# Optimization experiments

Hardware: AMD Instinct MI355X
Metric: run time of the kernel (lower is better)

## Reference

```python
import jax, jax.numpy as jnp
import numpy as np

DIM = 96
D_STATE = 16
EXPAND = 2
D_INNER = EXPAND * DIM
DT_RANK = (DIM + 15) // 16  # 6
B, H, W = 2, 64, 64
K = 4  # scan directions


def _ln(x, w, b, eps=1e-5):
    mu = x.mean(-1, keepdims=True)
    var = x.var(-1, keepdims=True)
    return (x - mu) / jnp.sqrt(var + eps) * w + b


def setup_inputs() -> dict:
    key = jax.random.key(0)
    ks = jax.random.split(key, 10)
    f = jnp.float32
    x = jax.random.normal(ks[0], (B, H, W, DIM), dtype=f)
    y = jax.random.normal(ks[1], (B, H, W, DIM), dtype=f)
    inp = {
        'x': x,
        'y': y,
        'ln_w': jnp.ones((DIM,), f),
        'ln_b': jnp.zeros((DIM,), f),
        'in_proj_w': jax.random.normal(ks[2], (2 * D_INNER, DIM), f) * 0.05,
        'conv_w': jax.random.normal(ks[3], (D_INNER, 1, 3, 3), f) * 0.1,
        'conv_b': jnp.zeros((D_INNER,), f),
        'x_proj_w': jax.random.normal(ks[4], (K, DT_RANK + 2 * D_STATE, D_INNER), f) * 0.05,
        'dt_w': jax.random.normal(ks[5], (K, D_INNER, DT_RANK), f) * 0.1,
        'dt_b': jax.random.normal(ks[6], (K, D_INNER), f) * 0.1,
        'A_log': jnp.broadcast_to(jnp.log(jnp.arange(1, D_STATE + 1, dtype=f)), (K, D_INNER, D_STATE)),
        'Ds': jnp.ones((K, D_INNER), f),
        'out_norm_w': jnp.ones((D_INNER,), f),
        'out_norm_b': jnp.zeros((D_INNER,), f),
        'out_proj_w': jax.random.normal(ks[7], (DIM, D_INNER), f) * 0.05,
    }
    return inp


def _fwd(x, y, ln_w, ln_b, in_proj_w, conv_w, conv_b, x_proj_w, dt_w, dt_b,
         A_log, Ds, out_norm_w, out_norm_b, out_proj_w):
    Bsz, Hh, Ww, C = x.shape
    Din = conv_w.shape[0]
    N = A_log.shape[-1]
    R = dt_w.shape[-1]
    L = Hh * Ww

    diff = jnp.abs(x - y)                       # TemporalSpectrumBlock abs-diff
    h = _ln(diff, ln_w, ln_b)                   # VSSBlock ln_1
    xz = h @ in_proj_w.T                        # (B,H,W,2*Din)
    xm, z = jnp.split(xz, 2, axis=-1)
    xm = xm.transpose(0, 3, 1, 2)               # (B,Din,H,W)
    xm = jax.lax.conv_general_dilated(
        xm, conv_w, (1, 1), 'SAME', feature_group_count=Din,
        dimension_numbers=('NCHW', 'OIHW', 'NCHW')) + conv_b[None, :, None, None]
    xm = jax.nn.silu(xm)

    # 4-directional sequences (B,4,Din,L)
    x0 = xm.reshape(Bsz, Din, L)
    x1 = xm.transpose(0, 1, 3, 2).reshape(Bsz, Din, L)
    xs = jnp.stack([x0, x1], axis=1)
    xs = jnp.concatenate([xs, jnp.flip(xs, axis=-1)], axis=1)

    x_dbl = jnp.einsum('bkdl,kcd->bkcl', xs, x_proj_w)
    dts, Bs, Cs = jnp.split(x_dbl, [R, R + N], axis=2)   # (B,4,R,L),(B,4,N,L),(B,4,N,L)
    dts = jnp.einsum('bkrl,kdr->bkdl', dts, dt_w)
    delta = jax.nn.softplus(dts + dt_b[None, :, :, None])  # (B,4,Din,L)

    A = -jnp.exp(A_log)                                    # (4,Din,N)
    dA = jnp.exp(delta[..., None] * A[None, :, :, None, :])          # (B,4,Din,L,N)
    dBu = delta[..., None] * Bs.transpose(0, 1, 3, 2)[:, :, None] * xs[..., None]

    dA_t = dA.transpose(3, 0, 1, 2, 4)    # (L,B,4,Din,N)
    dBu_t = dBu.transpose(3, 0, 1, 2, 4)
    C_t = Cs.transpose(3, 0, 1, 2)        # (L,B,4,N)
    h0 = jnp.zeros((Bsz, 4, Din, N), dtype=x.dtype)

    def step(hc, inp):
        a, bu, c = inp
        hc = a * hc + bu
        yv = jnp.einsum('bkdn,bkn->bkd', hc, c)
        return hc, yv

    _, ys = jax.lax.scan(step, h0, (dA_t, dBu_t, C_t))    # (L,B,4,Din)
    ys = ys.transpose(1, 2, 3, 0)                          # (B,4,Din,L)
    out_y = ys + Ds[None, :, :, None] * xs

    inv_y = jnp.flip(out_y[:, 2:4], axis=-1)
    wh_y = out_y[:, 1].reshape(Bsz, Din, Ww, Hh).transpose(0, 1, 3, 2).reshape(Bsz, Din, L)
    invwh_y = inv_y[:, 1].reshape(Bsz, Din, Ww, Hh).transpose(0, 1, 3, 2).reshape(Bsz, Din, L)
    yc = out_y[:, 0] + inv_y[:, 0] + wh_y + invwh_y        # (B,Din,L)
    yc = yc.transpose(0, 2, 1).reshape(Bsz, Hh, Ww, Din)

    yn = _ln(yc, out_norm_w, out_norm_b)
    out = (yn * jax.nn.silu(z)) @ out_proj_w.T
    return diff + out                                      # residual around the block


def reference(x, y, ln_w, ln_b, in_proj_w, conv_w, conv_b, x_proj_w, dt_w, dt_b,
              A_log, Ds, out_norm_w, out_norm_b, out_proj_w):
    return _fwd(x, y, ln_w, ln_b, in_proj_w, conv_w, conv_b, x_proj_w, dt_w, dt_b,
                A_log, Ds, out_norm_w, out_norm_b, out_proj_w)
```

## Files before the change

### kernel.cpp

```cpp
#include <hip/hip_runtime.h>
#include <math.h>

#define DIMC 96
#define DIN  192
#define NST  16
#define RNK  6
#define KD   4
#define HH   64
#define WWD  64
#define LL   4096
#define BB   2
#define NC   64
#define CH   64

__device__ __forceinline__ int pos_of(int k, int l) {
    int t = ((l & 63) << 6) | (l >> 6);
    switch (k) {
        case 0: return l;
        case 1: return t;
        case 2: return LL - 1 - l;
        default: return ((((LL-1-l) & 63) << 6) | ((LL-1-l) >> 6));
    }
}

__device__ __forceinline__ float silu_f(float v) {
    return v / (1.f + expf(-v));
}

__global__ __launch_bounds__(256) void k0_prep(
    const float* __restrict__ Win, const float* __restrict__ Wout,
    const float* __restrict__ xpw,
    float* __restrict__ WinT, float* __restrict__ WoutT, float* __restrict__ xpwT)
{
    int idx = blockIdx.x*256 + threadIdx.x;
    int stride = gridDim.x*256;
    for (int i = idx; i < 96*384; i += stride) {
        int j = i / 384, o = i - j*384;
        WinT[i] = Win[o*96 + j];
    }
    for (int i = idx; i < 192*96; i += stride) {
        int j = i / 96, o = i - j*96;
        WoutT[i] = Wout[o*192 + j];
    }
    for (int i = idx; i < 4*192*40; i += stride) {
        int kk = i / 7680; int rem = i - kk*7680;
        int j = rem / 40, c = rem - j*40;
        xpwT[i] = (c < RNK + 2*NST) ? xpw[((size_t)kk*(RNK+2*NST) + c)*DIN + j] : 0.f;
    }
}

__global__ __launch_bounds__(256) void k1_ln_inproj(
    const float* __restrict__ x, const float* __restrict__ y,
    const float* __restrict__ lnw, const float* __restrict__ lnb,
    const float* __restrict__ WinT,
    float* __restrict__ diff, float* __restrict__ xm, float* __restrict__ zbuf)
{
    __shared__ float hT[96*36];
    __shared__ float wl[96*132];
    __shared__ float mu_s[32], rs_s[32];
    int t = threadIdx.x;
    int p0 = blockIdx.x * 32;

    #pragma unroll
    for (int s = 0; s < 12; s++) {
        int i = t + 256*s;
        float v = fabsf(x[(size_t)p0*96 + i] - y[(size_t)p0*96 + i]);
        diff[(size_t)p0*96 + i] = v;
        int pos = i / 96, ch = i - pos*96;
        hT[ch*36 + pos] = v;
    }
    __syncthreads();
    {
        int tg = t & 7, pos = t >> 3;
        float s1 = 0.f, s2 = 0.f;
        #pragma unroll
        for (int m = 0; m < 12; m++) {
            float v = hT[(tg + 8*m)*36 + pos];
            s1 += v; s2 += v*v;
        }
        s1 += __shfl_down(s1, 4, 8); s2 += __shfl_down(s2, 4, 8);
        s1 += __shfl_down(s1, 2, 8); s2 += __shfl_down(s2, 2, 8);
        s1 += __shfl_down(s1, 1, 8); s2 += __shfl_down(s2, 1, 8);
        if (tg == 0) {
            float mu = s1 * (1.f/96.f);
            float var = s2 * (1.f/96.f) - mu*mu;
            mu_s[pos] = mu; rs_s[pos] = rsqrtf(var + 1e-5f);
        }
    }
    __syncthreads();
    #pragma unroll
    for (int s = 0; s < 12; s++) {
        int i = t + 256*s;
        int pos = i / 96, ch = i - pos*96;
        float v = hT[ch*36 + pos];
        hT[ch*36 + pos] = (v - mu_s[pos]) * rs_s[pos] * lnw[ch] + lnb[ch];
    }

    int o2 = t & 31, pg = t >> 5;
    for (int ot = 0; ot < 3; ot++) {
        __syncthreads();
        #pragma unroll
        for (int s = 0; s < 48; s++) {
            int i = t + 256*s;
            int j = i >> 7, ol = i & 127;
            wl[j*132 + ol] = WinT[j*384 + ot*128 + ol];
        }
        __syncthreads();
        float acc[4][4];
        #pragma unroll
        for (int a = 0; a < 4; a++)
            #pragma unroll
            for (int c = 0; c < 4; c++) acc[a][c] = 0.f;
        #pragma unroll 4
        for (int j = 0; j < 96; j++) {
            float wv[4], hv[4];
            *(float4*)wv = *(const float4*)&wl[j*132 + 4*o2];
            *(float4*)hv = *(const float4*)&hT[j*36 + 4*pg];
            #pragma unroll
            for (int pi = 0; pi < 4; pi++)
                #pragma unroll
                for (int c = 0; c < 4; c++) acc[pi][c] += hv[pi] * wv[c];
        }
        #pragma unroll
        for (int pi = 0; pi < 4; pi++) {
            int pos = p0 + 4*pg + pi;
            float4 val = make_float4(acc[pi][0], acc[pi][1], acc[pi][2], acc[pi][3]);
            int og = ot*128 + 4*o2;
            if (og < 192) *(float4*)&xm[(size_t)pos*192 + og] = val;
            else          *(float4*)&zbuf[(size_t)pos*192 + (og - 192)] = val;
        }
    }
}

__global__ __launch_bounds__(192) void k2_conv(
    const float* __restrict__ xm, const float* __restrict__ cw,
    const float* __restrict__ cb, float* __restrict__ xconv)
{
    int p = blockIdx.x;
    int d = threadIdx.x;
    int b = p >> 12;
    int l = p & (LL - 1);
    int hh = l >> 6, ww = l & 63;
    float acc = cb[d];
    const float* wd = cw + d*9;
    #pragma unroll
    for (int di = -1; di <= 1; di++) {
        int h2 = hh + di;
        if ((unsigned)h2 < HH) {
            #pragma unroll
            for (int dj = -1; dj <= 1; dj++) {
                int w2 = ww + dj;
                if ((unsigned)w2 < WWD)
                    acc += wd[(di+1)*3 + (dj+1)] * xm[((size_t)b*LL + h2*WWD + w2)*DIN + d];
            }
        }
    }
    xconv[(size_t)p*DIN + d] = silu_f(acc);
}

__global__ __launch_bounds__(256) void k3_xproj(
    const float* __restrict__ xconv, const float* __restrict__ xpwT,
    const float* __restrict__ dtw, const float* __restrict__ dtb,
    float* __restrict__ delta, float* __restrict__ Bs, float* __restrict__ Cs)
{
    __shared__ float uT[192*36];
    __shared__ float wx[192*40 + 64];
    __shared__ float xdl[32*40];
    int t = threadIdx.x;
    int blk = blockIdx.x;
    int tile = blk & 127, bk = blk >> 7;
    int k = bk & 3, b = bk >> 2;
    int c0 = tile*32;

    #pragma unroll
    for (int s = 0; s < 24; s++) {
        int i = t + 256*s;
        int pos = i / 192, ch = i - pos*192;
        int pp = pos_of(k, c0 + pos);
        uT[ch*36 + pos] = xconv[((size_t)b*LL + pp)*DIN + ch];
    }
    #pragma unroll
    for (int s = 0; s < 30; s++) {
        int i = t + 256*s;
        wx[i] = xpwT[(size_t)k*7680 + i];
    }
    __syncthreads();

    int pq = t & 7, cg = t >> 3;
    float a0[4] = {0,0,0,0}, a1[4] = {0,0,0,0};
    #pragma unroll 4
    for (int j = 0; j < 192; j++) {
        float uv[4];
        *(float4*)uv = *(const float4*)&uT[j*36 + 4*pq];
        float w0 = wx[j*40 + cg];
        float w1 = wx[j*40 + cg + 32];
        #pragma unroll
        for (int pi = 0; pi < 4; pi++) { a0[pi] += uv[pi]*w0; a1[pi] += uv[pi]*w1; }
    }
    #pragma unroll
    for (int pi = 0; pi < 4; pi++) {
        xdl[(4*pq + pi)*40 + cg] = a0[pi];
        if (cg < 8) xdl[(4*pq + pi)*40 + cg + 32] = a1[pi];
    }
    __syncthreads();

    if (t < 192) {
        int d = t;
        float w6[RNK];
        #pragma unroll
        for (int r = 0; r < RNK; r++) w6[r] = dtw[((size_t)k*DIN + d)*RNK + r];
        float bias = dtb[k*DIN + d];
        for (int pp = 0; pp < 32; pp++) {
            float acc = bias;
            #pragma unroll
            for (int r = 0; r < RNK; r++) acc += xdl[pp*40 + r] * w6[r];
            float sp = (acc > 20.f) ? acc : log1pf(expf(acc));
            delta[((size_t)bk*LL + c0 + pp)*DIN + d] = sp;
        }
    } else {
        int q = t - 192;
        int pp = q >> 1, half = q & 1;
        #pragma unroll
        for (int n8 = 0; n8 < 8; n8++) {
            int n = half*8 + n8;
            Bs[((size_t)bk*LL + c0 + pp)*NST + n] = xdl[pp*40 + RNK + n];
            Cs[((size_t)bk*LL + c0 + pp)*NST + n] = xdl[pp*40 + RNK + NST + n];
        }
    }
}

__global__ __launch_bounds__(192) void k4_scanA(
    const float* __restrict__ xconv, const float* __restrict__ delta,
    const float* __restrict__ BsArr, const float* __restrict__ A_log,
    float* __restrict__ P, float* __restrict__ Q)
{
    int blk = blockIdx.x;
    int c  = blk & (NC - 1);
    int bk = blk >> 6;
    int k  = bk & 3;
    int b  = bk >> 2;
    int d  = threadIdx.x;
    __shared__ float sB[CH][NST];
    for (int i = d; i < CH*NST; i += DIN) {
        int step = i >> 4, n = i & 15;
        sB[step][n] = BsArr[((size_t)bk*LL + c*CH + step)*NST + n];
    }
    float A[NST];
    #pragma unroll
    for (int n = 0; n < NST; n++) A[n] = -expf(A_log[((size_t)k*DIN + d)*NST + n]);
    __syncthreads();

    float h[NST], p[NST];
    #pragma unroll
    for (int n = 0; n < NST; n++) { h[n] = 0.f; p[n] = 1.f; }

    for (int step = 0; step < CH; step++) {
        int l = c*CH + step;
        float dl = delta[((size_t)bk*LL + l)*DIN + d];
        float uu = xconv[((size_t)b*LL + pos_of(k, l))*DIN + d];
        float du = dl * uu;
        #pragma unroll
        for (int n = 0; n < NST; n++) {
            float a = __expf(dl * A[n]);
            h[n] = a*h[n] + du*sB[step][n];
            p[n] *= a;
        }
    }
    size_t base = (size_t)blk*NST*DIN + d;
    #pragma unroll
    for (int n = 0; n < NST; n++) { P[base + n*DIN] = p[n]; Q[base + n*DIN] = h[n]; }
}

__global__ __launch_bounds__(256) void k5_scanB(
    const float* __restrict__ P, float* __restrict__ Q)
{
    int idx = blockIdx.x*256 + threadIdx.x;
    if (idx >= BB*KD*NST*DIN) return;
    int d = idx % DIN;
    int rest = idx / DIN;
    int n = rest % NST; rest /= NST;
    int k = rest % KD;
    int b = rest / KD;
    size_t base = ((((size_t)(b*KD + k))*NC)*NST + n)*DIN + d;
    size_t stride = (size_t)NST*DIN;
    float h = 0.f;
    for (int c = 0; c < NC; c++) {
        float p = P[base + c*stride];
        float q = Q[base + c*stride];
        Q[base + c*stride] = h;
        h = p*h + q;
    }
}

__global__ __launch_bounds__(192) void k6_scanC(
    const float* __restrict__ xconv, const float* __restrict__ delta,
    const float* __restrict__ BsArr, const float* __restrict__ CsArr,
    const float* __restrict__ A_log, const float* __restrict__ Ds,
    const float* __restrict__ Q, float* __restrict__ outy)
{
    int blk = blockIdx.x;
    int c  = blk & (NC - 1);
    int bk = blk >> 6;
    int k  = bk & 3;
    int b  = bk >> 2;
    int d  = threadIdx.x;
    __shared__ float sB[CH][NST];
    __shared__ float sC[CH][NST];
    for (int i = d; i < CH*NST; i += DIN) {
        int step = i >> 4, n = i & 15;
        sB[step][n] = BsArr[((size_t)bk*LL + c*CH + step)*NST + n];
        sC[step][n] = CsArr[((size_t)bk*LL + c*CH + step)*NST + n];
    }
    float A[NST];
    #pragma unroll
    for (int n = 0; n < NST; n++) A[n] = -expf(A_log[((size_t)k*DIN + d)*NST + n]);
    float h[NST];
    size_t base = (size_t)blk*NST*DIN + d;
    #pragma unroll
    for (int n = 0; n < NST; n++) h[n] = Q[base + n*DIN];
    float Dv = Ds[k*DIN + d];
    __syncthreads();

    for (int step = 0; step < CH; step++) {
        int l = c*CH + step;
        float dl = delta[((size_t)bk*LL + l)*DIN + d];
        float uu = xconv[((size_t)b*LL + pos_of(k, l))*DIN + d];
        float du = dl * uu;
        float yv = 0.f;
        #pragma unroll
        for (int n = 0; n < NST; n++) {
            float a = __expf(dl * A[n]);
            h[n] = a*h[n] + du*sB[step][n];
            yv += h[n] * sC[step][n];
        }
        outy[((size_t)bk*LL + l)*DIN + d] = yv + Dv*uu;
    }
}

__global__ __launch_bounds__(256) void k7_out(
    const float* __restrict__ outy, const float* __restrict__ zbuf,
    const float* __restrict__ diff, const float* __restrict__ onw,
    const float* __restrict__ onb, const float* __restrict__ WoutT,
    float* __restrict__ out)
{
    __shared__ float gT[192*36];
    __shared__ float wl[192*96];
    __shared__ float mu_s[32], rs_s[32];
    int t = threadIdx.x;
    int p0 = blockIdx.x*32;
    int b = p0 >> 12;
    int l0 = p0 & (LL - 1);

    #pragma unroll
    for (int s = 0; s < 72; s++) {
        int i = t + 256*s;
        wl[i] = WoutT[i];
    }
    #pragma unroll
    for (int s = 0; s < 24; s++) {
        int i = t + 256*s;
        int pos = i / 192, ch = i - pos*192;
        int l = l0 + pos;
        int tl = ((l & 63) << 6) | (l >> 6);
        float yc = outy[(((size_t)(b*KD + 0))*LL + l)*DIN + ch]
                 + outy[(((size_t)(b*KD + 2))*LL + (LL-1-l))*DIN + ch]
                 + outy[(((size_t)(b*KD + 1))*LL + tl)*DIN + ch]
                 + outy[(((size_t)(b*KD + 3))*LL + (LL-1-tl))*DIN + ch];
        gT[ch*36 + pos] = yc;
    }
    __syncthreads();
    {
        int tg = t & 7, pos = t >> 3;
        float s1 = 0.f, s2 = 0.f;
        #pragma unroll
        for (int m = 0; m < 24; m++) {
            float v = gT[(tg + 8*m)*36 + pos];
            s1 += v; s2 += v*v;
        }
        s1 += __shfl_down(s1, 4, 8); s2 += __shfl_down(s2, 4, 8);
        s1 += __shfl_down(s1, 2, 8); s2 += __shfl_down(s2, 2, 8);
        s1 += __shfl_down(s1, 1, 8); s2 += __shfl_down(s2, 1, 8);
        if (tg == 0) {
            float mu = s1 * (1.f/192.f);
            float var = s2 * (1.f/192.f) - mu*mu;
            mu_s[pos] = mu; rs_s[pos] = rsqrtf(var + 1e-5f);
        }
    }
    __syncthreads();
    #pragma unroll
    for (int s = 0; s < 24; s++) {
        int i = t + 256*s;
        int pos = i / 192, ch = i - pos*192;
        float v = gT[ch*36 + pos];
        float yn = (v - mu_s[pos]) * rs_s[pos] * onw[ch] + onb[ch];
        float z = zbuf[(size_t)(p0 + pos)*DIN + ch];
        gT[ch*36 + pos] = yn * silu_f(z);
    }
    __syncthreads();

    int o1 = t & 31, pg = t >> 5;
    float acc[4][3];
    #pragma unroll
    for (int a = 0; a < 4; a++) { acc[a][0] = 0.f; acc[a][1] = 0.f; acc[a][2] = 0.f; }
    #pragma unroll 4
    for (int j = 0; j < 192; j++) {
        float hv[4];
        *(float4*)hv = *(const float4*)&gT[j*36 + 4*pg];
        float w0 = wl[j*96 + o1];
        float w1 = wl[j*96 + o1 + 32];
        float w2 = wl[j*96 + o1 + 64];
        #pragma unroll
        for (int pi = 0; pi < 4; pi++) {
            acc[pi][0] += hv[pi]*w0;
            acc[pi][1] += hv[pi]*w1;
            acc[pi][2] += hv[pi]*w2;
        }
    }
    #pragma unroll
    for (int pi = 0; pi < 4; pi++) {
        size_t p = (size_t)(p0 + 4*pg + pi);
        out[p*DIMC + o1]      = acc[pi][0] + diff[p*DIMC + o1];
        out[p*DIMC + o1 + 32] = acc[pi][1] + diff[p*DIMC + o1 + 32];
        out[p*DIMC + o1 + 64] = acc[pi][2] + diff[p*DIMC + o1 + 64];
    }
}

extern "C" void kernel_launch(void* const* d_in, const int* in_sizes, int n_in,
                              void* d_out, int out_size, void* d_ws, size_t ws_size,
                              hipStream_t stream)
{
    const float* x       = (const float*)d_in[0];
    const float* y       = (const float*)d_in[1];
    const float* ln_w    = (const float*)d_in[2];
    const float* ln_b    = (const float*)d_in[3];
    const float* in_proj = (const float*)d_in[4];
    const float* conv_w  = (const float*)d_in[5];
    const float* conv_b  = (const float*)d_in[6];
    const float* x_proj  = (const float*)d_in[7];
    const float* dt_w    = (const float*)d_in[8];
    const float* dt_b    = (const float*)d_in[9];
    const float* A_log   = (const float*)d_in[10];
    const float* Ds      = (const float*)d_in[11];
    const float* onw     = (const float*)d_in[12];
    const float* onb     = (const float*)d_in[13];
    const float* out_w   = (const float*)d_in[14];
    float* out = (float*)d_out;

    float* ws    = (float*)d_ws;
    float* diff  = ws;
    float* zbuf  = diff  + 786432;
    float* xm    = zbuf  + 1572864;
    float* xconv = xm    + 1572864;
    float* delta = xconv + 1572864;
    float* Bs    = delta + 6291456;
    float* Cs    = Bs    + 524288;
    float* outy  = Cs    + 524288;
    float* Pbuf  = outy  + 6291456;
    float* Qbuf  = Pbuf  + 1572864;
    float* WinT  = Qbuf  + 1572864;
    float* WoutT = WinT  + 36864;
    float* xpwT  = WoutT + 18432;

    const int BL = BB * LL;

    hipLaunchKernelGGL(k0_prep, dim3(144), dim3(256), 0, stream,
                       in_proj, out_w, x_proj, WinT, WoutT, xpwT);
    hipLaunchKernelGGL(k1_ln_inproj, dim3(BL/32), dim3(256), 0, stream,
                       x, y, ln_w, ln_b, WinT, diff, xm, zbuf);
    hipLaunchKernelGGL(k2_conv, dim3(BL), dim3(DIN), 0, stream,
                       xm, conv_w, conv_b, xconv);
    hipLaunchKernelGGL(k3_xproj, dim3(BB*KD*128), dim3(256), 0, stream,
                       xconv, xpwT, dt_w, dt_b, delta, Bs, Cs);
    hipLaunchKernelGGL(k4_scanA, dim3(BB*KD*NC), dim3(DIN), 0, stream,
                       xconv, delta, Bs, A_log, Pbuf, Qbuf);
    hipLaunchKernelGGL(k5_scanB, dim3((BB*KD*NST*DIN + 255)/256), dim3(256), 0, stream,
                       Pbuf, Qbuf);
    hipLaunchKernelGGL(k6_scanC, dim3(BB*KD*NC), dim3(DIN), 0, stream,
                       xconv, delta, Bs, Cs, A_log, Ds, Qbuf, outy);
    hipLaunchKernelGGL(k7_out, dim3(BL/32), dim3(256), 0, stream,
                       outy, zbuf, diff, onw, onb, WoutT, out);
}
```

Before: 298.0 us.

## Fuse delta projection into scan kernels and restructure projection GEMMs

The x_proj kernel now computes only the 38 projection outputs per position in natural (unpermuted) order into a compact XDB buffer. The scan kernels gather those outputs through the direction permutation and recompute delta = softplus(dt_w·x + b) on the fly. This removes the large per-direction delta, B and C buffers and the global traffic that goes with them. The in_proj and out_proj GEMMs are also retiled to 64-position tiles, with each wave reading weights straight from global memory in uniform loads instead of staging them in LDS. The cost is repeated softplus and exp work in both scan passes, plus scattered gathers of XDB.

New measurement: 362.9 us. 21.8% more time.

```diff
diff --git a/kernel.cpp b/kernel.cpp
--- a/kernel.cpp
+++ b/kernel.cpp
@@ -12,6 +12,7 @@
 #define BB   2
 #define NC   64
 #define CH   64
+#define CPK  48
 
 __device__ __forceinline__ int pos_of(int k, int l) {
     int t = ((l & 63) << 6) | (l >> 6);
@@ -30,7 +31,7 @@
 __global__ __launch_bounds__(256) void k0_prep(
     const float* __restrict__ Win, const float* __restrict__ Wout,
     const float* __restrict__ xpw,
-    float* __restrict__ WinT, float* __restrict__ WoutT, float* __restrict__ xpwT)
+    float* __restrict__ WinT, float* __restrict__ WoutT, float* __restrict__ wT3)
 {
     int idx = blockIdx.x*256 + threadIdx.x;
     int stride = gridDim.x*256;
@@ -42,94 +43,82 @@
         int j = i / 96, o = i - j*96;
         WoutT[i] = Wout[o*192 + j];
     }
-    for (int i = idx; i < 4*192*40; i += stride) {
-        int kk = i / 7680; int rem = i - kk*7680;
-        int j = rem / 40, c = rem - j*40;
-        xpwT[i] = (c < RNK + 2*NST) ? xpw[((size_t)kk*(RNK+2*NST) + c)*DIN + j] : 0.f;
-    }
-}
-
-__global__ __launch_bounds__(256) void k1_ln_inproj(
+    for (int i = idx; i < KD*192*CPK; i += stride) {
+        int kk = i / (192*CPK); int rem = i - kk*192*CPK;
+        int j = rem / CPK, c = rem - j*CPK;
+        wT3[i] = (c < RNK + 2*NST) ? xpw[((size_t)kk*(RNK+2*NST) + c)*DIN + j] : 0.f;
+    }
+}
+
+__global__ __launch_bounds__(1024) void k1_ln_inproj(
     const float* __restrict__ x, const float* __restrict__ y,
     const float* __restrict__ lnw, const float* __restrict__ lnb,
     const float* __restrict__ WinT,
     float* __restrict__ diff, float* __restrict__ xm, float* __restrict__ zbuf)
 {
-    __shared__ float hT[96*36];
-    __shared__ float wl[96*132];
-    __shared__ float mu_s[32], rs_s[32];
+    __shared__ float hT[96*65];
+    __shared__ float ps1[16*64], ps2[16*64];
+    __shared__ float mus[64], rss[64];
     int t = threadIdx.x;
-    int p0 = blockIdx.x * 32;
-
-    #pragma unroll
-    for (int s = 0; s < 12; s++) {
-        int i = t + 256*s;
+    int ptile = blockIdx.x >> 1, cgrp = blockIdx.x & 1;
+    int p0 = ptile*64;
+
+    #pragma unroll
+    for (int s = 0; s < 6; s++) {
+        int i = t + 1024*s;
         float v = fabsf(x[(size_t)p0*96 + i] - y[(size_t)p0*96 + i]);
-        diff[(size_t)p0*96 + i] = v;
+        if (cgrp == 0) diff[(size_t)p0*96 + i] = v;
         int pos = i / 96, ch = i - pos*96;
-        hT[ch*36 + pos] = v;
+        hT[ch*65 + pos] = v;
     }
     __syncthreads();
     {
-        int tg = t & 7, pos = t >> 3;
+        int pos = t & 63, part = t >> 6;
         float s1 = 0.f, s2 = 0.f;
         #pragma unroll
-        for (int m = 0; m < 12; m++) {
-            float v = hT[(tg + 8*m)*36 + pos];
+        for (int m = 0; m < 6; m++) {
+            float v = hT[(part*6 + m)*65 + pos];
             s1 += v; s2 += v*v;
         }
-        s1 += __shfl_down(s1, 4, 8); s2 += __shfl_down(s2, 4, 8);
-        s1 += __shfl_down(s1, 2, 8); s2 += __shfl_down(s2, 2, 8);
-        s1 += __shfl_down(s1, 1, 8); s2 += __shfl_down(s2, 1, 8);
-        if (tg == 0) {
-            float mu = s1 * (1.f/96.f);
-            float var = s2 * (1.f/96.f) - mu*mu;
-            mu_s[pos] = mu; rs_s[pos] = rsqrtf(var + 1e-5f);
-        }
-    }
-    __syncthreads();
-    #pragma unroll
-    for (int s = 0; s < 12; s++) {
-        int i = t + 256*s;
+        ps1[part*64 + pos] = s1; ps2[part*64 + pos] = s2;
+    }
+    __syncthreads();
+    if (t < 64) {
+        float S1 = 0.f, S2 = 0.f;
+        #pragma unroll
+        for (int i = 0; i < 16; i++) { S1 += ps1[i*64 + t]; S2 += ps2[i*64 + t]; }
+        float mu = S1 * (1.f/96.f);
+        float var = S2 * (1.f/96.f) - mu*mu;
+        mus[t] = mu; rss[t] = rsqrtf(var + 1e-5f);
+    }
+    __syncthreads();
+    #pragma unroll
+    for (int s = 0; s < 6; s++) {
+        int i = t + 1024*s;
         int pos = i / 96, ch = i - pos*96;
-        float v = hT[ch*36 + pos];
-        hT[ch*36 + pos] = (v - mu_s[pos]) * rs_s[pos] * lnw[ch] + lnb[ch];
-    }
-
-    int o2 = t & 31, pg = t >> 5;
-    for (int ot = 0; ot < 3; ot++) {
-        __syncthreads();
-        #pragma unroll
-        for (int s = 0; s < 48; s++) {
-            int i = t + 256*s;
-            int j = i >> 7, ol = i & 127;
-            wl[j*132 + ol] = WinT[j*384 + ot*128 + ol];
-        }
-        __syncthreads();
-        float acc[4][4];
-        #pragma unroll
-        for (int a = 0; a < 4; a++)
-            #pragma unroll
-            for (int c = 0; c < 4; c++) acc[a][c] = 0.f;
-        #pragma unroll 4
-        for (int j = 0; j < 96; j++) {
-            float wv[4], hv[4];
-            *(float4*)wv = *(const float4*)&wl[j*132 + 4*o2];
-            *(float4*)hv = *(const float4*)&hT[j*36 + 4*pg];
-            #pragma unroll
-            for (int pi = 0; pi < 4; pi++)
-                #pragma unroll
-                for (int c = 0; c < 4; c++) acc[pi][c] += hv[pi] * wv[c];
-        }
-        #pragma unroll
-        for (int pi = 0; pi < 4; pi++) {
-            int pos = p0 + 4*pg + pi;
-            float4 val = make_float4(acc[pi][0], acc[pi][1], acc[pi][2], acc[pi][3]);
-            int og = ot*128 + 4*o2;
-            if (og < 192) *(float4*)&xm[(size_t)pos*192 + og] = val;
-            else          *(float4*)&zbuf[(size_t)pos*192 + (og - 192)] = val;
-        }
-    }
+        hT[ch*65 + pos] = (hT[ch*65 + pos] - mus[pos]) * rss[pos] * lnw[ch] + lnb[ch];
+    }
+    __syncthreads();
+
+    int w = __builtin_amdgcn_readfirstlane(t >> 6);
+    int lane = t & 63;
+    int c0 = cgrp*192 + w*12;
+    const float* wp = WinT + c0;
+    float acc[12];
+    #pragma unroll
+    for (int cc = 0; cc < 12; cc++) acc[cc] = 0.f;
+    #pragma unroll 2
+    for (int j = 0; j < 96; j++) {
+        float u = hT[j*65 + lane];
+        const float* wrow = wp + j*384;
+        #pragma unroll
+        for (int cc = 0; cc < 12; cc++) acc[cc] += u * wrow[cc];
+    }
+    size_t p = (size_t)(p0 + lane);
+    float* dst = (c0 < 192) ? (xm + p*192 + c0) : (zbuf + p*192 + (c0 - 192));
+    #pragma unroll
+    for (int q = 0; q < 3; q++)
+        *(float4*)&dst[4*q] = make_float4(acc[4*q], acc[4*q+1], acc[4*q+2], acc[4*q+3]);
 }
 
 __global__ __launch_bounds__(192) void k2_conv(
@@ -158,80 +147,49 @@
     xconv[(size_t)p*DIN + d] = silu_f(acc);
 }
 
-__global__ __launch_bounds__(256) void k3_xproj(
-    const float* __restrict__ xconv, const float* __restrict__ xpwT,
+__global__ __launch_bounds__(512) void k3_xproj(
+    const float* __restrict__ xconv, const float* __restrict__ wT3,
+    float* __restrict__ XDB)
+{
+    __shared__ float uT[192*65];
+    int t = threadIdx.x;
+    int ptile = blockIdx.x >> 1, wgrp = blockIdx.x & 1;
+    int p0 = ptile*64;
+
+    #pragma unroll
+    for (int s = 0; s < 24; s++) {
+        int i = t + 512*s;
+        int pos = i / 192, ch = i - pos*192;
+        uT[ch*65 + pos] = xconv[(size_t)(p0 + pos)*192 + ch];
+    }
+    __syncthreads();
+
+    int w = __builtin_amdgcn_readfirstlane(t >> 6);
+    int slot = wgrp*8 + w;
+    int k = slot >> 2, cq = slot & 3;
+    int lane = t & 63;
+    int c0 = cq*12;
+    const float* wp = wT3 + (size_t)k*192*CPK + c0;
+    float acc[12];
+    #pragma unroll
+    for (int cc = 0; cc < 12; cc++) acc[cc] = 0.f;
+    #pragma unroll 2
+    for (int j = 0; j < 192; j++) {
+        float u = uT[j*65 + lane];
+        const float* wrow = wp + j*CPK;
+        #pragma unroll
+        for (int cc = 0; cc < 12; cc++) acc[cc] += u * wrow[cc];
+    }
+    float* dst = XDB + (size_t)(p0 + lane)*(KD*CPK) + k*CPK + c0;
+    #pragma unroll
+    for (int q = 0; q < 3; q++)
+        *(float4*)&dst[4*q] = make_float4(acc[4*q], acc[4*q+1], acc[4*q+2], acc[4*q+3]);
+}
+
+__global__ __launch_bounds__(192) void k4_scanA(
+    const float* __restrict__ xconv, const float* __restrict__ XDB,
     const float* __restrict__ dtw, const float* __restrict__ dtb,
-    float* __restrict__ delta, float* __restrict__ Bs, float* __restrict__ Cs)
-{
-    __shared__ float uT[192*36];
-    __shared__ float wx[192*40 + 64];
-    __shared__ float xdl[32*40];
-    int t = threadIdx.x;
-    int blk = blockIdx.x;
-    int tile = blk & 127, bk = blk >> 7;
-    int k = bk & 3, b = bk >> 2;
-    int c0 = tile*32;
-
-    #pragma unroll
-    for (int s = 0; s < 24; s++) {
-        int i = t + 256*s;
-        int pos = i / 192, ch = i - pos*192;
-        int pp = pos_of(k, c0 + pos);
-        uT[ch*36 + pos] = xconv[((size_t)b*LL + pp)*DIN + ch];
-    }
-    #pragma unroll
-    for (int s = 0; s < 30; s++) {
-        int i = t + 256*s;
-        wx[i] = xpwT[(size_t)k*7680 + i];
-    }
-    __syncthreads();
-
-    int pq = t & 7, cg = t >> 3;
-    float a0[4] = {0,0,0,0}, a1[4] = {0,0,0,0};
-    #pragma unroll 4
-    for (int j = 0; j < 192; j++) {
-        float uv[4];
-        *(float4*)uv = *(const float4*)&uT[j*36 + 4*pq];
-        float w0 = wx[j*40 + cg];
-        float w1 = wx[j*40 + cg + 32];
-        #pragma unroll
-        for (int pi = 0; pi < 4; pi++) { a0[pi] += uv[pi]*w0; a1[pi] += uv[pi]*w1; }
-    }
-    #pragma unroll
-    for (int pi = 0; pi < 4; pi++) {
-        xdl[(4*pq + pi)*40 + cg] = a0[pi];
-        if (cg < 8) xdl[(4*pq + pi)*40 + cg + 32] = a1[pi];
-    }
-    __syncthreads();
-
-    if (t < 192) {
-        int d = t;
-        float w6[RNK];
-        #pragma unroll
-        for (int r = 0; r < RNK; r++) w6[r] = dtw[((size_t)k*DIN + d)*RNK + r];
-        float bias = dtb[k*DIN + d];
-        for (int pp = 0; pp < 32; pp++) {
-            float acc = bias;
-            #pragma unroll
-            for (int r = 0; r < RNK; r++) acc += xdl[pp*40 + r] * w6[r];
-            float sp = (acc > 20.f) ? acc : log1pf(expf(acc));
-            delta[((size_t)bk*LL + c0 + pp)*DIN + d] = sp;
-        }
-    } else {
-        int q = t - 192;
-        int pp = q >> 1, half = q & 1;
-        #pragma unroll
-        for (int n8 = 0; n8 < 8; n8++) {
-            int n = half*8 + n8;
-            Bs[((size_t)bk*LL + c0 + pp)*NST + n] = xdl[pp*40 + RNK + n];
-            Cs[((size_t)bk*LL + c0 + pp)*NST + n] = xdl[pp*40 + RNK + NST + n];
-        }
-    }
-}
-
-__global__ __launch_bounds__(192) void k4_scanA(
-    const float* __restrict__ xconv, const float* __restrict__ delta,
-    const float* __restrict__ BsArr, const float* __restrict__ A_log,
+    const float* __restrict__ A_log,
     float* __restrict__ P, float* __restrict__ Q)
 {
     int blk = blockIdx.x;
@@ -240,35 +198,43 @@
     int k  = bk & 3;
     int b  = bk >> 2;
     int d  = threadIdx.x;
-    __shared__ float sB[CH][NST];
-    for (int i = d; i < CH*NST; i += DIN) {
-        int step = i >> 4, n = i & 15;
-        sB[step][n] = BsArr[((size_t)bk*LL + c*CH + step)*NST + n];
-    }
+    __shared__ float sXD[CH*49];
+    for (int i = d; i < CH*48; i += DIN) {
+        int step = i / 48, cc = i - step*48;
+        int pp = pos_of(k, c*CH + step);
+        sXD[step*49 + cc] = XDB[(size_t)(b*LL + pp)*(KD*CPK) + k*CPK + cc];
+    }
+    float dw[RNK];
+    #pragma unroll
+    for (int r = 0; r < RNK; r++) dw[r] = dtw[((size_t)k*DIN + d)*RNK + r];
+    float bias = dtb[k*DIN + d];
     float A[NST];
     #pragma unroll
     for (int n = 0; n < NST; n++) A[n] = -expf(A_log[((size_t)k*DIN + d)*NST + n]);
     __syncthreads();
 
-    float h[NST], p[NST];
-    #pragma unroll
-    for (int n = 0; n < NST; n++) { h[n] = 0.f; p[n] = 1.f; }
+    float h[NST], pr[NST];
+    #pragma unroll
+    for (int n = 0; n < NST; n++) { h[n] = 0.f; pr[n] = 1.f; }
 
     for (int step = 0; step < CH; step++) {
         int l = c*CH + step;
-        float dl = delta[((size_t)bk*LL + l)*DIN + d];
+        float dl = bias;
+        #pragma unroll
+        for (int r = 0; r < RNK; r++) dl += sXD[step*49 + r] * dw[r];
+        dl = (dl > 20.f) ? dl : log1pf(expf(dl));
         float uu = xconv[((size_t)b*LL + pos_of(k, l))*DIN + d];
         float du = dl * uu;
         #pragma unroll
         for (int n = 0; n < NST; n++) {
             float a = __expf(dl * A[n]);
-            h[n] = a*h[n] + du*sB[step][n];
-            p[n] *= a;
+            h[n] = a*h[n] + du*sXD[step*49 + 6 + n];
+            pr[n] *= a;
         }
     }
     size_t base = (size_t)blk*NST*DIN + d;
     #pragma unroll
-    for (int n = 0; n < NST; n++) { P[base + n*DIN] = p[n]; Q[base + n*DIN] = h[n]; }
+    for (int n = 0; n < NST; n++) { P[base + n*DIN] = pr[n]; Q[base + n*DIN] = h[n]; }
 }
 
 __global__ __launch_bounds__(256) void k5_scanB(
@@ -293,8 +259,8 @@
 }
 
 __global__ __launch_bounds__(192) void k6_scanC(
-    const float* __restrict__ xconv, const float* __restrict__ delta,
-    const float* __restrict__ BsArr, const float* __restrict__ CsArr,
+    const float* __restrict__ xconv, const float* __restrict__ XDB,
+    const float* __restrict__ dtw, const float* __restrict__ dtb,
     const float* __restrict__ A_log, const float* __restrict__ Ds,
     const float* __restrict__ Q, float* __restrict__ outy)
 {
@@ -304,13 +270,16 @@
     int k  = bk & 3;
     int b  = bk >> 2;
     int d  = threadIdx.x;
-    __shared__ float sB[CH][NST];
-    __shared__ float sC[CH][NST];
-    for (int i = d; i < CH*NST; i += DIN) {
-        int step = i >> 4, n = i & 15;
-        sB[step][n] = BsArr[((size_t)bk*LL + c*CH + step)*NST + n];
-        sC[step][n] = CsArr[((size_t)bk*LL + c*CH + step)*NST + n];
-    }
+    __shared__ float sXD[CH*49];
+    for (int i = d; i < CH*48; i += DIN) {
+        int step = i / 48, cc = i - step*48;
+        int pp = pos_of(k, c*CH + step);
+        sXD[step*49 + cc] = XDB[(size_t)(b*LL + pp)*(KD*CPK) + k*CPK + cc];
+    }
+    float dw[RNK];
+    #pragma unroll
+    for (int r = 0; r < RNK; r++) dw[r] = dtw[((size_t)k*DIN + d)*RNK + r];
+    float bias = dtb[k*DIN + d];
     float A[NST];
     #pragma unroll
     for (int n = 0; n < NST; n++) A[n] = -expf(A_log[((size_t)k*DIN + d)*NST + n]);
@@ -323,15 +292,18 @@
 
     for (int step = 0; step < CH; step++) {
         int l = c*CH + step;
-        float dl = delta[((size_t)bk*LL + l)*DIN + d];
+        float dl = bias;
+        #pragma unroll
+        for (int r = 0; r < RNK; r++) dl += sXD[step*49 + r] * dw[r];
+        dl = (dl > 20.f) ? dl : log1pf(expf(dl));
         float uu = xconv[((size_t)b*LL + pos_of(k, l))*DIN + d];
         float du = dl * uu;
         float yv = 0.f;
         #pragma unroll
         for (int n = 0; n < NST; n++) {
             float a = __expf(dl * A[n]);
-            h[n] = a*h[n] + du*sB[step][n];
-            yv += h[n] * sC[step][n];
+            h[n] = a*h[n] + du*sXD[step*49 + 6 + n];
+            yv += h[n] * sXD[step*49 + 22 + n];
         }
         outy[((size_t)bk*LL + l)*DIN + d] = yv + Dv*uu;
     }
@@ -343,21 +315,17 @@
     const float* __restrict__ onb, const float* __restrict__ WoutT,
     float* __restrict__ out)
 {
-    __shared__ float gT[192*36];
-    __shared__ float wl[192*96];
-    __shared__ float mu_s[32], rs_s[32];
+    __shared__ float gT[192*65];
+    __shared__ float ps1[4*64], ps2[4*64];
+    __shared__ float mus[64], rss[64];
     int t = threadIdx.x;
-    int p0 = blockIdx.x*32;
+    int ptile = blockIdx.x >> 1, chalf = blockIdx.x & 1;
+    int p0 = ptile*64;
     int b = p0 >> 12;
     int l0 = p0 & (LL - 1);
 
     #pragma unroll
-    for (int s = 0; s < 72; s++) {
-        int i = t + 256*s;
-        wl[i] = WoutT[i];
-    }
-    #pragma unroll
-    for (int s = 0; s < 24; s++) {
+    for (int s = 0; s < 48; s++) {
         int i = t + 256*s;
         int pos = i / 192, ch = i - pos*192;
         int l = l0 + pos;
@@ -366,62 +334,59 @@
                  + outy[(((size_t)(b*KD + 2))*LL + (LL-1-l))*DIN + ch]
                  + outy[(((size_t)(b*KD + 1))*LL + tl)*DIN + ch]
                  + outy[(((size_t)(b*KD + 3))*LL + (LL-1-tl))*DIN + ch];
-        gT[ch*36 + pos] = yc;
+        gT[ch*65 + pos] = yc;
     }
     __syncthreads();
     {
-        int tg = t & 7, pos = t >> 3;
+        int pos = t & 63, part = t >> 6;
         float s1 = 0.f, s2 = 0.f;
         #pragma unroll
-        for (int m = 0; m < 24; m++) {
-            float v = gT[(tg + 8*m)*36 + pos];
+        for (int m = 0; m < 48; m++) {
+            float v = gT[(part*48 + m)*65 + pos];
             s1 += v; s2 += v*v;
         }
-        s1 += __shfl_down(s1, 4, 8); s2 += __shfl_down(s2, 4, 8);
-        s1 += __shfl_down(s1, 2, 8); s2 += __shfl_down(s2, 2, 8);
-        s1 += __shfl_down(s1, 1, 8); s2 += __shfl_down(s2, 1, 8);
-        if (tg == 0) {
-            float mu = s1 * (1.f/192.f);
-            float var = s2 * (1.f/192.f) - mu*mu;
-            mu_s[pos] = mu; rs_s[pos] = rsqrtf(var + 1e-5f);
-        }
-    }
-    __syncthreads();
-    #pragma unroll
-    for (int s = 0; s < 24; s++) {
+        ps1[part*64 + pos] = s1; ps2[part*64 + pos] = s2;
+    }
+    __syncthreads();
+    if (t < 64) {
+        float S1 = ps1[t] + ps1[64+t] + ps1[128+t] + ps1[192+t];
+        float S2 = ps2[t] + ps2[64+t] + ps2[128+t] + ps2[192+t];
+        float mu = S1 * (1.f/192.f);
+        float var = S2 * (1.f/192.f) - mu*mu;
+        mus[t] = mu; rss[t] = rsqrtf(var + 1e-5f);
+    }
+    __syncthreads();
+    #pragma unroll
+    for (int s = 0; s < 48; s++) {
         int i = t + 256*s;
         int pos = i / 192, ch = i - pos*192;
-        float v = gT[ch*36 + pos];
-        float yn = (v - mu_s[pos]) * rs_s[pos] * onw[ch] + onb[ch];
+        float v = gT[ch*65 + pos];
+        float yn = (v - mus[pos]) * rss[pos] * onw[ch] + onb[ch];
         float z = zbuf[(size_t)(p0 + pos)*DIN + ch];
-        gT[ch*36 + pos] = yn * silu_f(z);
-    }
-    __syncthreads();
-
-    int o1 = t & 31, pg = t >> 5;
-    float acc[4][3];
-    #pragma unroll
-    for (int a = 0; a < 4; a++) { acc[a][0] = 0.f; acc[a][1] = 0.f; acc[a][2] = 0.f; }
-    #pragma unroll 4
+        gT[ch*65 + pos] = yn * silu_f(z);
+    }
+    __syncthreads();
+
+    int w = __builtin_amdgcn_readfirstlane(t >> 6);
+    int lane = t & 63;
+    int c0 = chalf*48 + w*12;
+    const float* wp = WoutT + c0;
+    float acc[12];
+    #pragma unroll
+    for (int cc = 0; cc < 12; cc++) acc[cc] = 0.f;
+    #pragma unroll 2
     for (int j = 0; j < 192; j++) {
-        float hv[4];
-        *(float4*)hv = *(const float4*)&gT[j*36 + 4*pg];
-        float w0 = wl[j*96 + o1];
-        float w1 = wl[j*96 + o1 + 32];
-        float w2 = wl[j*96 + o1 + 64];
-        #pragma unroll
-        for (int pi = 0; pi < 4; pi++) {
-            acc[pi][0] += hv[pi]*w0;
-            acc[pi][1] += hv[pi]*w1;
-            acc[pi][2] += hv[pi]*w2;
-        }
-    }
-    #pragma unroll
-    for (int pi = 0; pi < 4; pi++) {
-        size_t p = (size_t)(p0 + 4*pg + pi);
-        out[p*DIMC + o1]      = acc[pi][0] + diff[p*DIMC + o1];
-        out[p*DIMC + o1 + 32] = acc[pi][1] + diff[p*DIMC + o1 + 32];
-        out[p*DIMC + o1 + 64] = acc[pi][2] + diff[p*DIMC + o1 + 64];
+        float u = gT[j*65 + lane];
+        const float* wrow = wp + j*96;
+        #pragma unroll
+        for (int cc = 0; cc < 12; cc++) acc[cc] += u * wrow[cc];
+    }
+    size_t p = (size_t)(p0 + lane);
+    #pragma unroll
+    for (int q = 0; q < 3; q++) {
+        float4 dv = *(const float4*)&diff[p*96 + c0 + 4*q];
+        *(float4*)&out[p*96 + c0 + 4*q] =
+            make_float4(acc[4*q] + dv.x, acc[4*q+1] + dv.y, acc[4*q+2] + dv.z, acc[4*q+3] + dv.w);
     }
 }
 
@@ -451,32 +416,30 @@
     float* zbuf  = diff  + 786432;
     float* xm    = zbuf  + 1572864;
     float* xconv = xm    + 1572864;
-    float* delta = xconv + 1572864;
-    float* Bs    = delta + 6291456;
-    float* Cs    = Bs    + 524288;
-    float* outy  = Cs    + 524288;
+    float* XDB   = xconv + 1572864;
+    float* outy  = XDB   + 1572864;
     float* Pbuf  = outy  + 6291456;
     float* Qbuf  = Pbuf  + 1572864;
     float* WinT  = Qbuf  + 1572864;
     float* WoutT = WinT  + 36864;
-    float* xpwT  = WoutT + 18432;
+    float* wT3   = WoutT + 18432;
 
     const int BL = BB * LL;
 
     hipLaunchKernelGGL(k0_prep, dim3(144), dim3(256), 0, stream,
-                       in_proj, out_w, x_proj, WinT, WoutT, xpwT);
-    hipLaunchKernelGGL(k1_ln_inproj, dim3(BL/32), dim3(256), 0, stream,
+                       in_proj, out_w, x_proj, WinT, WoutT, wT3);
+    hipLaunchKernelGGL(k1_ln_inproj, dim3(BL/64*2), dim3(1024), 0, stream,
                        x, y, ln_w, ln_b, WinT, diff, xm, zbuf);
     hipLaunchKernelGGL(k2_conv, dim3(BL), dim3(DIN), 0, stream,
                        xm, conv_w, conv_b, xconv);
-    hipLaunchKernelGGL(k3_xproj, dim3(BB*KD*128), dim3(256), 0, stream,
-                       xconv, xpwT, dt_w, dt_b, delta, Bs, Cs);
+    hipLaunchKernelGGL(k3_xproj, dim3(BL/64*2), dim3(512), 0, stream,
+                       xconv, wT3, XDB);
     hipLaunchKernelGGL(k4_scanA, dim3(BB*KD*NC), dim3(DIN), 0, stream,
-                       xconv, delta, Bs, A_log, Pbuf, Qbuf);
+                       xconv, XDB, dt_w, dt_b, A_log, Pbuf, Qbuf);
     hipLaunchKernelGGL(k5_scanB, dim3((BB*KD*NST*DIN + 255)/256), dim3(256), 0, stream,
                        Pbuf, Qbuf);
     hipLaunchKernelGGL(k6_scanC, dim3(BB*KD*NC), dim3(DIN), 0, stream,
-                       xconv, delta, Bs, Cs, A_log, Ds, Qbuf, outy);
-    hipLaunchKernelGGL(k7_out, dim3(BL/32), dim3(256), 0, stream,
+                       xconv, XDB, dt_w, dt_b, A_log, Ds, Qbuf, outy);
+    hipLaunchKernelGGL(k7_out, dim3(BL/64*2), dim3(256), 0, stream,
                        outy, zbuf, diff, onw, onb, WoutT, out);
 }
```
